# Optimization experiments

Hardware: AMD Instinct MI355X
Metric: run time of the kernel (lower is better)

The kernel has to match this reference:

```python
import jax, jax.numpy as jnp
import numpy as np

B, T, C = 2, 4096, 768
H = 12
HD = C // H  # 64

def setup_inputs() -> dict:
    key = jax.random.key(0)
    k1, k2, k3 = jax.random.split(key, 3)
    scale_in = 1.0 / np.sqrt(C)
    return {
        "x": jax.random.normal(k1, (B, T, C), dtype=jnp.float32),
        "w_qkv": jax.random.normal(k2, (C, 3 * C), dtype=jnp.float32) * scale_in,
        "b_qkv": jnp.zeros((3 * C,), dtype=jnp.float32),
        "w_proj": jax.random.normal(k3, (C, C), dtype=jnp.float32) * scale_in,
        "b_proj": jnp.zeros((C,), dtype=jnp.float32),
    }

def reference(x, w_qkv, b_qkv, w_proj, b_proj):
    # Dropout in eval mode (identity), matching module.eval().
    Bx, Tx, Cx = x.shape
    qkv = x @ w_qkv + b_qkv                      # [B,T,3C]
    q, k, v = jnp.split(qkv, 3, axis=-1)
    def to_heads(t):
        return t.reshape(Bx, Tx, H, HD).transpose(0, 2, 1, 3)  # [B,H,T,hd]
    q, k, v = to_heads(q), to_heads(k), to_heads(v)
    att = jnp.einsum('bhqd,bhkd->bhqk', q, k) / jnp.sqrt(jnp.float32(HD))
    causal = jnp.tril(jnp.ones((Tx, Tx), dtype=bool))
    att = jnp.where(causal[None, None], att, -jnp.inf)
    att = jax.nn.softmax(att, axis=-1)
    y = jnp.einsum('bhqk,bhkd->bhqd', att, v)    # [B,H,T,hd]
    y = y.transpose(0, 2, 1, 3).reshape(Bx, Tx, Cx)
    return y @ w_proj + b_proj
```

## Files before the change

### kernel.cpp

```cpp
#include <hip/hip_runtime.h>


#define TSEQ 4096
#define NH 12
#define CDIM 768

typedef __bf16 bf16;
typedef __attribute__((ext_vector_type(8))) __bf16 bf16x8;
typedef __attribute__((ext_vector_type(4))) __bf16 bf16x4;
typedef __attribute__((ext_vector_type(4))) float f32x4;

__device__ __forceinline__ void gload16(const void* g, void* l) {
  __builtin_amdgcn_global_load_lds(
      (const __attribute__((address_space(1))) void*)g,
      (__attribute__((address_space(3))) void*)l, 16, 0, 0);
}

__device__ __forceinline__ float fexp2(float x) {
  return __builtin_amdgcn_exp2f(x);
}

#define MAX3(a, b, c) fmaxf(fmaxf((a), (b)), (c))

__global__ void convert_x_kernel(const float* __restrict__ x,
                                 bf16* __restrict__ xb, int n) {
  int i = (blockIdx.x * blockDim.x + threadIdx.x) * 4;
  if (i < n) {
    float4 v = *(const float4*)(x + i);
    bf16x4 o;
    o[0] = (bf16)v.x; o[1] = (bf16)v.y; o[2] = (bf16)v.z; o[3] = (bf16)v.w;
    *(bf16x4*)(xb + i) = o;
  }
}

__global__ void transpose_w_kernel(const float* __restrict__ src,
                                   bf16* __restrict__ dst, int R, int Cc) {
  __shared__ float tile[32][33];
  int tx = threadIdx.x, ty = threadIdx.y;
  int c0 = blockIdx.x * 32, r0 = blockIdx.y * 32;
#pragma unroll
  for (int i = 0; i < 4; ++i)
    tile[ty + i * 8][tx] = src[(size_t)(r0 + ty + i * 8) * Cc + c0 + tx];
  __syncthreads();
#pragma unroll
  for (int i = 0; i < 4; ++i)
    dst[(size_t)(c0 + ty + i * 8) * R + r0 + tx] = (bf16)tile[tx][ty + i * 8];
}

template <int MODE>
__global__ __launch_bounds__(256) void gemm_kernel(
    const bf16* __restrict__ A, const bf16* __restrict__ BT,
    const float* __restrict__ bias, bf16* __restrict__ qk_out,
    bf16* __restrict__ vT_out, float* __restrict__ c_out) {
  constexpr int K = 768;
  __shared__ alignas(16) bf16 As[128 * 64];
  __shared__ alignas(16) bf16 Bs[128 * 64];
  const int t = threadIdx.x;
  const int l = t & 63, w = t >> 6;
  const int l15 = l & 15, lg = l >> 4;
  const int nwg = gridDim.x * gridDim.y;
  int id = blockIdx.y * gridDim.x + blockIdx.x;
  id = (id & 7) * (nwg >> 3) + (id >> 3);
  const int m0 = (id / gridDim.x) << 7, n0 = (id % gridDim.x) << 7;
  const int wr = w >> 1, wc = w & 1;

  f32x4 acc[4][4] = {};

  const int r0 = t >> 3;
  const int kb8 = (((t & 7) ^ (r0 & 7)) << 3);
  const bf16* Asrc = A + (size_t)(m0 + r0) * K + kb8;
  const bf16* Bsrc = BT + (size_t)(n0 + r0) * K + kb8;

  for (int kt = 0; kt < K / 64; ++kt) {
#pragma unroll
    for (int i = 0; i < 4; ++i)
      gload16(Asrc + kt * 64 + (size_t)i * 32 * K, (char*)As + w * 1024 + i * 4096);
#pragma unroll
    for (int i = 0; i < 4; ++i)
      gload16(Bsrc + kt * 64 + (size_t)i * 32 * K, (char*)Bs + w * 1024 + i * 4096);
    __syncthreads();
#pragma unroll
    for (int kk = 0; kk < 2; ++kk) {
      bf16x8 af[4], bfv[4];
#pragma unroll
      for (int m = 0; m < 4; ++m) {
        int r = (wr << 6) + (m << 4) + l15;
        int kb = (kk << 2) + lg;
        af[m] = *(const bf16x8*)((const char*)As + r * 128 + ((kb ^ (r & 7)) << 4));
      }
#pragma unroll
      for (int n = 0; n < 4; ++n) {
        int r = (wc << 6) + (n << 4) + l15;
        int kb = (kk << 2) + lg;
        bfv[n] = *(const bf16x8*)((const char*)Bs + r * 128 + ((kb ^ (r & 7)) << 4));
      }
#pragma unroll
      for (int m = 0; m < 4; ++m)
#pragma unroll
        for (int n = 0; n < 4; ++n)
          acc[m][n] = __builtin_amdgcn_mfma_f32_16x16x32_bf16(af[m], bfv[n],
                                                              acc[m][n], 0, 0, 0);
    }
    __syncthreads();
  }

#pragma unroll
  for (int m = 0; m < 4; ++m) {
    int row = m0 + (wr << 6) + (m << 4) + (lg << 2);
    int b = row >> 12, tt = row & 4095;
#pragma unroll
    for (int n = 0; n < 4; ++n) {
      int col = n0 + (wc << 6) + (n << 4) + l15;
      float bv = bias[col];
      if (MODE == 0) {
        if (col < 1536) {
          float sc = (col < 768) ? 0.18033688011112042f : 1.0f;
          bf16* dst = qk_out + (size_t)(b * TSEQ + tt) * 1536 + col;
#pragma unroll
          for (int j = 0; j < 4; ++j)
            dst[(size_t)j * 1536] = (bf16)((acc[m][n][j] + bv) * sc);
        } else {
          int nl = col - 1536;
          bf16* dst = vT_out +
              ((size_t)(b * NH + (nl >> 6)) * 64 + (nl & 63)) * TSEQ + tt;
#pragma unroll
          for (int j = 0; j < 4; ++j) dst[j] = (bf16)(acc[m][n][j] + bv);
        }
      } else {
        float* dst = c_out + (size_t)row * 768 + col;
#pragma unroll
        for (int j = 0; j < 4; ++j) dst[(size_t)j * 768] = acc[m][n][j] + bv;
      }
    }
  }
}

__global__ __launch_bounds__(256) void attn_kernel(
    const bf16* __restrict__ qk,
    const bf16* __restrict__ vT,
    bf16* __restrict__ y,
    bf16* __restrict__ opart,
    float* __restrict__ mlb) {
  __shared__ alignas(16) char lds[24576];
  const int t = threadIdx.x;
  const int l = t & 63, w = t >> 6;
  const int l15 = l & 15, lg = l >> 4;

  const int rk = blockIdx.x;
  const int xcd = rk & 7, s = rk >> 3;
  const int bh = xcd * 3 + (s % 3);
  const int j = s / 3;
  int qb, kt0, kt1, half, split;
  if (j < 64) {
    int i = j >> 1;
    qb = 63 - i; half = j & 1; split = 1;
    int nk = qb + 1, nh0 = (nk + 1) >> 1;
    kt0 = half ? nh0 : 0;
    kt1 = half ? nk : nh0;
  } else {
    qb = 95 - j; half = 0; split = 0;
    kt0 = 0; kt1 = qb + 1;
  }
  const int b = bh / NH, h = bh % NH;
  const bf16* qbase = qk + (size_t)b * TSEQ * 1536 + h * 64;
  const bf16* kbase = qbase + 768;
  const bf16* vbase = vT + (size_t)bh * 64 * TSEQ;

  const int r0 = t >> 3;
  const int kb8 = (((t & 7) ^ (r0 & 7)) << 3);
  const int q0 = qb << 6;
  const int qw = q0 + (w << 4);

  const int swz = l15 & 7;
  int koff[2];
  koff[0] = l15 * 128 + ((lg ^ swz) << 4);
  koff[1] = l15 * 128 + (((4 + lg) ^ swz) << 4);
  char* const preg = lds + w * 2048;
  const char* par[2] = {preg + koff[0], preg + koff[1]};
  char* pwa[4];
#pragma unroll
  for (int m = 0; m < 4; ++m)
    pwa[m] = preg + l15 * 128 + ((((m << 5) + (lg << 3)) ^ (swz << 4)));

#pragma unroll
  for (int i = 0; i < 2; ++i) {
    gload16(qbase + (size_t)(q0 + i * 32 + r0) * 1536 + kb8,
            lds + w * 1024 + i * 4096);
    gload16(kbase + (size_t)(kt0 * 64 + i * 32 + r0) * 1536 + kb8,
            lds + 0x2000 + w * 1024 + i * 4096);
    gload16(vbase + (size_t)(i * 32 + r0) * TSEQ + kt0 * 64 + kb8,
            lds + 0x4000 + w * 1024 + i * 4096);
  }
  const bf16* ksrc = kbase + (size_t)((kt0 + 1) * 64 + r0) * 1536 + kb8;
  const bf16* vsrc = vbase + (size_t)r0 * TSEQ + (kt0 + 1) * 64 + kb8;
  int4 kr0, kr1, vr0, vr1;
  if (kt0 + 1 < kt1) {
    kr0 = *(const int4*)(ksrc);
    kr1 = *(const int4*)(ksrc + (size_t)32 * 1536);
    vr0 = *(const int4*)(vsrc);
    vr1 = *(const int4*)(vsrc + (size_t)32 * TSEQ);
    ksrc += (size_t)64 * 1536;
    vsrc += 64;
  }
  __syncthreads();

  bf16x8 qf[2];
#pragma unroll
  for (int kk = 0; kk < 2; ++kk) {
    int r = (w << 4) + l15;
    int kb = (kk << 2) + lg;
    qf[kk] = *(const bf16x8*)(lds + r * 128 + ((kb ^ (r & 7)) << 4));
  }

  f32x4 o[4] = {};
  float mrun = -__builtin_inff();
  float lrun = 0.f;

  for (int kt = kt0; kt < kt1; ++kt) {
    const int kv0 = kt << 6;

    f32x4 s4[4] = {};
    __builtin_amdgcn_s_setprio(1);
#pragma unroll
    for (int kk = 0; kk < 2; ++kk) {
#pragma unroll
      for (int m = 0; m < 4; ++m) {
        bf16x8 kf = *(const bf16x8*)(lds + 0x2000 + koff[kk] + m * 2048);
        s4[m] = __builtin_amdgcn_mfma_f32_16x16x32_bf16(kf, qf[kk], s4[m], 0, 0, 0);
      }
    }
    __builtin_amdgcn_s_setprio(0);

    if (kv0 + 63 > qw) {
      int q = qw + l15;
#pragma unroll
      for (int m = 0; m < 4; ++m) {
        int kvr = kv0 + (m << 4) + (lg << 2);
#pragma unroll
        for (int jj = 0; jj < 4; ++jj)
          if (kvr + jj > q) s4[m][jj] = -__builtin_inff();
      }
    }
    float t0 = MAX3(s4[0][0], s4[0][1], s4[0][2]);
    float t1 = MAX3(s4[0][3], s4[1][0], s4[1][1]);
    float t2 = MAX3(s4[1][2], s4[1][3], s4[2][0]);
    float t3 = MAX3(s4[2][1], s4[2][2], s4[2][3]);
    float t4 = MAX3(s4[3][0], s4[3][1], s4[3][2]);
    float cmax = MAX3(MAX3(t0, t1, s4[3][3]), fmaxf(t2, t3), t4);
    cmax = fmaxf(cmax, __shfl_xor(cmax, 16));
    cmax = fmaxf(cmax, __shfl_xor(cmax, 32));
    if (__any(cmax > mrun + 8.f)) {
      float mnew = fmaxf(mrun, cmax);
      float alpha = fexp2(mrun - mnew);
      mrun = mnew;
      lrun *= alpha;
#pragma unroll
      for (int jj = 0; jj < 4; ++jj) {
        int rr = (lg << 2) + jj;
        float a = __shfl(alpha, (l & 48) | rr);
#pragma unroll
        for (int no = 0; no < 4; ++no) o[no][jj] *= a;
      }
    }
    float ps = 0.f;
#pragma unroll
    for (int m = 0; m < 4; ++m)
#pragma unroll
      for (int jj = 0; jj < 4; ++jj) {
        float pv = fexp2(s4[m][jj] - mrun);
        s4[m][jj] = pv;
        ps += pv;
      }
    ps += __shfl_xor(ps, 16);
    ps += __shfl_xor(ps, 32);
    lrun += ps;
#pragma unroll
    for (int m = 0; m < 4; ++m) {
      bf16x4 pv;
#pragma unroll
      for (int jj = 0; jj < 4; ++jj) pv[jj] = (bf16)s4[m][jj];
      *(bf16x4*)(pwa[m]) = pv;
    }
    __builtin_amdgcn_s_setprio(1);
#pragma unroll
    for (int kk = 0; kk < 2; ++kk) {
      bf16x8 pa = *(const bf16x8*)(par[kk]);
#pragma unroll
      for (int no = 0; no < 4; ++no) {
        bf16x8 vb = *(const bf16x8*)(lds + 0x4000 + koff[kk] + no * 2048);
        o[no] = __builtin_amdgcn_mfma_f32_16x16x32_bf16(pa, vb, o[no], 0, 0, 0);
      }
    }
    __builtin_amdgcn_s_setprio(0);

    if (kt + 1 < kt1) {
      __syncthreads();
      *(int4*)(lds + 0x2000 + t * 16) = kr0;
      *(int4*)(lds + 0x2000 + 4096 + t * 16) = kr1;
      *(int4*)(lds + 0x4000 + t * 16) = vr0;
      *(int4*)(lds + 0x4000 + 4096 + t * 16) = vr1;
      if (kt + 2 < kt1) {
        kr0 = *(const int4*)(ksrc);
        kr1 = *(const int4*)(ksrc + (size_t)32 * 1536);
        vr0 = *(const int4*)(vsrc);
        vr1 = *(const int4*)(vsrc + (size_t)32 * TSEQ);
        ksrc += (size_t)64 * 1536;
        vsrc += 64;
      }
      __syncthreads();
    }
  }

  if (!split) {
#pragma unroll
    for (int jj = 0; jj < 4; ++jj) {
      int rr = (lg << 2) + jj;
      float lv = __shfl(lrun, (l & 48) | rr);
      float linv = 1.0f / lv;
      int qrow = qw + rr;
      size_t base = ((size_t)(b * TSEQ + qrow)) * 768 + h * 64;
#pragma unroll
      for (int no = 0; no < 4; ++no)
        y[base + (no << 4) + l15] = (bf16)(o[no][jj] * linv);
    }
  } else {
    const int sb2 = (bh * 32 + (qb - 32)) * 2 + half;
#pragma unroll
    for (int jj = 0; jj < 4; ++jj) {
      int rr = (lg << 2) + jj;
      float lv = __shfl(lrun, (l & 48) | rr);
      float linv = 1.0f / lv;
      int r = (w << 4) + rr;
      size_t base = ((size_t)sb2 * 64 + r) * 64;
#pragma unroll
      for (int no = 0; no < 4; ++no)
        opart[base + (no << 4) + l15] = (bf16)(o[no][jj] * linv);
    }
    if (l < 16) {
      size_t mi = ((size_t)sb2 * 64 + (w << 4) + l) * 2;
      mlb[mi] = mrun;
      mlb[mi + 1] = lrun;
    }
  }
}

__global__ void combine_kernel(const bf16* __restrict__ op,
                               const float* __restrict__ ml,
                               bf16* __restrict__ y) {
  int g = blockIdx.x * 256 + threadIdx.x;
  int d4 = (g & 15) << 2;
  int rid = g >> 4;
  int rr = rid & 63;
  int sb = rid >> 6;
  int bh = sb >> 5, qb = 32 + (sb & 31);
  int b = bh / NH, h = bh % NH;
  size_t m0i = ((size_t)(sb * 2) * 64 + rr) * 2;
  size_t m1i = ((size_t)(sb * 2 + 1) * 64 + rr) * 2;
  float m0 = ml[m0i], l0 = ml[m0i + 1];
  float m1 = ml[m1i], l1 = ml[m1i + 1];
  float M = fmaxf(m0, m1);
  float w0 = fexp2(m0 - M) * l0, w1 = fexp2(m1 - M) * l1;
  float inv = 1.f / (w0 + w1);
  w0 *= inv; w1 *= inv;
  const bf16* o0 = op + (((size_t)(sb * 2) * 64 + rr) * 64 + d4);
  const bf16* o1 = op + (((size_t)(sb * 2 + 1) * 64 + rr) * 64 + d4);
  bf16x4 a = *(const bf16x4*)o0, c = *(const bf16x4*)o1;
  bf16x4 out;
#pragma unroll
  for (int jj = 0; jj < 4; ++jj)
    out[jj] = (bf16)(w0 * (float)a[jj] + w1 * (float)c[jj]);
  int qrow = (qb << 6) + rr;
  *(bf16x4*)(y + ((size_t)(b * TSEQ + qrow)) * 768 + h * 64 + d4) = out;
}

extern "C" void kernel_launch(void* const* d_in, const int* in_sizes, int n_in,
                              void* d_out, int out_size, void* d_ws,
                              size_t ws_size, hipStream_t stream) {
  const float* x = (const float*)d_in[0];
  const float* w_qkv = (const float*)d_in[1];
  const float* b_qkv = (const float*)d_in[2];
  const float* w_proj = (const float*)d_in[3];
  const float* b_proj = (const float*)d_in[4];
  float* out = (float*)d_out;
  char* ws = (char*)d_ws;

  bf16* xb     = (bf16*)(ws);
  bf16* wqkvT  = (bf16*)(ws + 12582912);
  bf16* wprojT = (bf16*)(ws + 16121856);
  bf16* qkbuf  = (bf16*)(ws + 17301504);
  bf16* vTbuf  = (bf16*)(ws + 42467328);
  bf16* ybuf   = (bf16*)(ws + 55050240);
  float* mlb   = (float*)(ws + 67633152);

  convert_x_kernel<<<6144, 256, 0, stream>>>(x, xb, 2 * TSEQ * CDIM);
  transpose_w_kernel<<<dim3(72, 24), dim3(32, 8), 0, stream>>>(w_qkv, wqkvT, 768, 2304);
  transpose_w_kernel<<<dim3(24, 24), dim3(32, 8), 0, stream>>>(w_proj, wprojT, 768, 768);
  gemm_kernel<0><<<dim3(18, 64), 256, 0, stream>>>(xb, wqkvT, b_qkv, qkbuf, vTbuf, nullptr);
  attn_kernel<<<2304, 256, 0, stream>>>(qkbuf, vTbuf, ybuf, xb, mlb);
  combine_kernel<<<3072, 256, 0, stream>>>(xb, mlb, ybuf);
  gemm_kernel<1><<<dim3(6, 64), 256, 0, stream>>>(ybuf, wprojT, b_proj, nullptr, nullptr, out);
}
```

Baseline: 247.7 us.

## Enlarge attention query tile to 128 rows with two 16-row subtiles per wave

After: 268.6 us. 8.4% more time.

```diff
diff --git a/kernel.cpp b/kernel.cpp
--- a/kernel.cpp
+++ b/kernel.cpp
@@ -135,13 +135,13 @@
   }
 }
 
-__global__ __launch_bounds__(256) void attn_kernel(
+__global__ __launch_bounds__(256, 4) void attn_kernel(
     const bf16* __restrict__ qk,
     const bf16* __restrict__ vT,
     bf16* __restrict__ y,
     bf16* __restrict__ opart,
     float* __restrict__ mlb) {
-  __shared__ alignas(16) char lds[24576];
+  __shared__ alignas(16) char lds[32768];
   const int t = threadIdx.x;
   const int l = t & 63, w = t >> 6;
   const int l15 = l & 15, lg = l >> 4;
@@ -151,15 +151,14 @@
   const int bh = xcd * 3 + (s % 3);
   const int j = s / 3;
   int qb, kt0, kt1, half, split;
-  if (j < 64) {
-    int i = j >> 1;
-    qb = 63 - i; half = j & 1; split = 1;
-    int nk = qb + 1, nh0 = (nk + 1) >> 1;
+  if (j < 32) {
+    qb = 31 - (j >> 1); half = j & 1; split = 1;
+    int nh0 = qb + 1;
     kt0 = half ? nh0 : 0;
-    kt1 = half ? nk : nh0;
+    kt1 = half ? 2 * qb + 2 : nh0;
   } else {
-    qb = 95 - j; half = 0; split = 0;
-    kt0 = 0; kt1 = qb + 1;
+    qb = 47 - j; half = 0; split = 0;
+    kt0 = 0; kt1 = 2 * qb + 2;
   }
   const int b = bh / NH, h = bh % NH;
   const bf16* qbase = qk + (size_t)b * TSEQ * 1536 + h * 64;
@@ -168,28 +167,29 @@
 
   const int r0 = t >> 3;
   const int kb8 = (((t & 7) ^ (r0 & 7)) << 3);
-  const int q0 = qb << 6;
-  const int qw = q0 + (w << 4);
+  const int q0 = qb << 7;
+  const int qwmax = q0 + (w << 5) + 31;
 
   const int swz = l15 & 7;
   int koff[2];
   koff[0] = l15 * 128 + ((lg ^ swz) << 4);
   koff[1] = l15 * 128 + (((4 + lg) ^ swz) << 4);
-  char* const preg = lds + w * 2048;
-  const char* par[2] = {preg + koff[0], preg + koff[1]};
-  char* pwa[4];
+  char* const preg = lds + w * 4096;
+  int so[4];
 #pragma unroll
   for (int m = 0; m < 4; ++m)
-    pwa[m] = preg + l15 * 128 + ((((m << 5) + (lg << 3)) ^ (swz << 4)));
-
-#pragma unroll
-  for (int i = 0; i < 2; ++i) {
+    so[m] = l15 * 128 + ((((m << 5) + (lg << 3)) ^ (swz << 4)));
+
+#pragma unroll
+  for (int i = 0; i < 4; ++i)
     gload16(qbase + (size_t)(q0 + i * 32 + r0) * 1536 + kb8,
             lds + w * 1024 + i * 4096);
+#pragma unroll
+  for (int i = 0; i < 2; ++i) {
     gload16(kbase + (size_t)(kt0 * 64 + i * 32 + r0) * 1536 + kb8,
-            lds + 0x2000 + w * 1024 + i * 4096);
+            lds + 0x4000 + w * 1024 + i * 4096);
     gload16(vbase + (size_t)(i * 32 + r0) * TSEQ + kt0 * 64 + kb8,
-            lds + 0x4000 + w * 1024 + i * 4096);
+            lds + 0x6000 + w * 1024 + i * 4096);
   }
   const bf16* ksrc = kbase + (size_t)((kt0 + 1) * 64 + r0) * 1536 + kb8;
   const bf16* vsrc = vbase + (size_t)r0 * TSEQ + (kt0 + 1) * 64 + kb8;
@@ -204,101 +204,137 @@
   }
   __syncthreads();
 
-  bf16x8 qf[2];
-#pragma unroll
-  for (int kk = 0; kk < 2; ++kk) {
-    int r = (w << 4) + l15;
-    int kb = (kk << 2) + lg;
-    qf[kk] = *(const bf16x8*)(lds + r * 128 + ((kb ^ (r & 7)) << 4));
-  }
-
-  f32x4 o[4] = {};
-  float mrun = -__builtin_inff();
-  float lrun = 0.f;
+  bf16x8 qf[2][2];
+#pragma unroll
+  for (int n = 0; n < 2; ++n)
+#pragma unroll
+    for (int kk = 0; kk < 2; ++kk) {
+      int r = (w << 5) + (n << 4) + l15;
+      int kb = (kk << 2) + lg;
+      qf[n][kk] = *(const bf16x8*)(lds + r * 128 + ((kb ^ (r & 7)) << 4));
+    }
+
+  f32x4 o[2][4] = {};
+  float mrun[2] = {0.f, 0.f};
+  float lrun[2] = {0.f, 0.f};
 
   for (int kt = kt0; kt < kt1; ++kt) {
     const int kv0 = kt << 6;
 
-    f32x4 s4[4] = {};
-    __builtin_amdgcn_s_setprio(1);
-#pragma unroll
-    for (int kk = 0; kk < 2; ++kk) {
-#pragma unroll
-      for (int m = 0; m < 4; ++m) {
-        bf16x8 kf = *(const bf16x8*)(lds + 0x2000 + koff[kk] + m * 2048);
-        s4[m] = __builtin_amdgcn_mfma_f32_16x16x32_bf16(kf, qf[kk], s4[m], 0, 0, 0);
-      }
-    }
-    __builtin_amdgcn_s_setprio(0);
-
-    if (kv0 + 63 > qw) {
-      int q = qw + l15;
-#pragma unroll
-      for (int m = 0; m < 4; ++m) {
-        int kvr = kv0 + (m << 4) + (lg << 2);
-#pragma unroll
-        for (int jj = 0; jj < 4; ++jj)
-          if (kvr + jj > q) s4[m][jj] = -__builtin_inff();
-      }
-    }
-    float t0 = MAX3(s4[0][0], s4[0][1], s4[0][2]);
-    float t1 = MAX3(s4[0][3], s4[1][0], s4[1][1]);
-    float t2 = MAX3(s4[1][2], s4[1][3], s4[2][0]);
-    float t3 = MAX3(s4[2][1], s4[2][2], s4[2][3]);
-    float t4 = MAX3(s4[3][0], s4[3][1], s4[3][2]);
-    float cmax = MAX3(MAX3(t0, t1, s4[3][3]), fmaxf(t2, t3), t4);
-    cmax = fmaxf(cmax, __shfl_xor(cmax, 16));
-    cmax = fmaxf(cmax, __shfl_xor(cmax, 32));
-    if (__any(cmax > mrun + 8.f)) {
-      float mnew = fmaxf(mrun, cmax);
-      float alpha = fexp2(mrun - mnew);
-      mrun = mnew;
-      lrun *= alpha;
-#pragma unroll
-      for (int jj = 0; jj < 4; ++jj) {
-        int rr = (lg << 2) + jj;
-        float a = __shfl(alpha, (l & 48) | rr);
-#pragma unroll
-        for (int no = 0; no < 4; ++no) o[no][jj] *= a;
-      }
-    }
-    float ps = 0.f;
-#pragma unroll
-    for (int m = 0; m < 4; ++m)
-#pragma unroll
-      for (int jj = 0; jj < 4; ++jj) {
-        float pv = fexp2(s4[m][jj] - mrun);
-        s4[m][jj] = pv;
-        ps += pv;
-      }
-    ps += __shfl_xor(ps, 16);
-    ps += __shfl_xor(ps, 32);
-    lrun += ps;
-#pragma unroll
-    for (int m = 0; m < 4; ++m) {
-      bf16x4 pv;
-#pragma unroll
-      for (int jj = 0; jj < 4; ++jj) pv[jj] = (bf16)s4[m][jj];
-      *(bf16x4*)(pwa[m]) = pv;
-    }
-    __builtin_amdgcn_s_setprio(1);
-#pragma unroll
-    for (int kk = 0; kk < 2; ++kk) {
-      bf16x8 pa = *(const bf16x8*)(par[kk]);
-#pragma unroll
-      for (int no = 0; no < 4; ++no) {
-        bf16x8 vb = *(const bf16x8*)(lds + 0x4000 + koff[kk] + no * 2048);
-        o[no] = __builtin_amdgcn_mfma_f32_16x16x32_bf16(pa, vb, o[no], 0, 0, 0);
-      }
-    }
-    __builtin_amdgcn_s_setprio(0);
+    if (kv0 <= qwmax) {
+      f32x4 s4[2][4];
+#pragma unroll
+      for (int n = 0; n < 2; ++n) {
+        float mi = -mrun[n];
+#pragma unroll
+        for (int m = 0; m < 4; ++m) {
+          s4[n][m][0] = mi; s4[n][m][1] = mi; s4[n][m][2] = mi; s4[n][m][3] = mi;
+        }
+      }
+      __builtin_amdgcn_s_setprio(1);
+#pragma unroll
+      for (int kk = 0; kk < 2; ++kk) {
+        bf16x8 kf[4];
+#pragma unroll
+        for (int m = 0; m < 4; ++m)
+          kf[m] = *(const bf16x8*)(lds + 0x4000 + koff[kk] + m * 2048);
+#pragma unroll
+        for (int m = 0; m < 4; ++m)
+#pragma unroll
+          for (int n = 0; n < 2; ++n)
+            s4[n][m] = __builtin_amdgcn_mfma_f32_16x16x32_bf16(
+                kf[m], qf[n][kk], s4[n][m], 0, 0, 0);
+      }
+      __builtin_amdgcn_s_setprio(0);
+
+      if (kv0 + 63 > q0 + (w << 5)) {
+#pragma unroll
+        for (int n = 0; n < 2; ++n) {
+          int qn = q0 + (w << 5) + (n << 4) + l15;
+#pragma unroll
+          for (int m = 0; m < 4; ++m) {
+            int kvr = kv0 + (m << 4) + (lg << 2);
+#pragma unroll
+            for (int jj = 0; jj < 4; ++jj)
+              if (kvr + jj > qn) s4[n][m][jj] = -__builtin_inff();
+          }
+        }
+      }
+      float cm[2];
+#pragma unroll
+      for (int n = 0; n < 2; ++n) {
+        float t0 = MAX3(s4[n][0][0], s4[n][0][1], s4[n][0][2]);
+        float t1 = MAX3(s4[n][0][3], s4[n][1][0], s4[n][1][1]);
+        float t2 = MAX3(s4[n][1][2], s4[n][1][3], s4[n][2][0]);
+        float t3 = MAX3(s4[n][2][1], s4[n][2][2], s4[n][2][3]);
+        float t4 = MAX3(s4[n][3][0], s4[n][3][1], s4[n][3][2]);
+        float c = MAX3(MAX3(t0, t1, s4[n][3][3]), fmaxf(t2, t3), t4);
+        c = fmaxf(c, __shfl_xor(c, 16));
+        cm[n] = fmaxf(c, __shfl_xor(c, 32));
+      }
+      if (__any((cm[0] > 8.f) || (cm[1] > 8.f))) {
+#pragma unroll
+        for (int n = 0; n < 2; ++n) {
+          float delta = fmaxf(cm[n], 0.f);
+          float alpha = fexp2(-delta);
+          mrun[n] += delta;
+          lrun[n] *= alpha;
+#pragma unroll
+          for (int jj = 0; jj < 4; ++jj) {
+            int rr = (lg << 2) + jj;
+            float a = __shfl(alpha, (l & 48) | rr);
+#pragma unroll
+            for (int no = 0; no < 4; ++no) o[n][no][jj] *= a;
+          }
+#pragma unroll
+          for (int m = 0; m < 4; ++m)
+#pragma unroll
+            for (int jj = 0; jj < 4; ++jj) s4[n][m][jj] -= delta;
+        }
+      }
+#pragma unroll
+      for (int n = 0; n < 2; ++n) {
+        float ps = 0.f;
+#pragma unroll
+        for (int m = 0; m < 4; ++m) {
+          bf16x4 pv;
+#pragma unroll
+          for (int jj = 0; jj < 4; ++jj) {
+            float p = fexp2(s4[n][m][jj]);
+            pv[jj] = (bf16)p;
+            ps += p;
+          }
+          *(bf16x4*)(preg + (n << 11) + so[m]) = pv;
+        }
+        ps += __shfl_xor(ps, 16);
+        ps += __shfl_xor(ps, 32);
+        lrun[n] += ps;
+      }
+      __builtin_amdgcn_s_setprio(1);
+#pragma unroll
+      for (int kk = 0; kk < 2; ++kk) {
+        bf16x8 vbv[4];
+#pragma unroll
+        for (int no = 0; no < 4; ++no)
+          vbv[no] = *(const bf16x8*)(lds + 0x6000 + koff[kk] + no * 2048);
+#pragma unroll
+        for (int n = 0; n < 2; ++n) {
+          bf16x8 pa = *(const bf16x8*)(preg + (n << 11) + koff[kk]);
+#pragma unroll
+          for (int no = 0; no < 4; ++no)
+            o[n][no] = __builtin_amdgcn_mfma_f32_16x16x32_bf16(
+                pa, vbv[no], o[n][no], 0, 0, 0);
+        }
+      }
+      __builtin_amdgcn_s_setprio(0);
+    }
 
     if (kt + 1 < kt1) {
       __syncthreads();
-      *(int4*)(lds + 0x2000 + t * 16) = kr0;
-      *(int4*)(lds + 0x2000 + 4096 + t * 16) = kr1;
-      *(int4*)(lds + 0x4000 + t * 16) = vr0;
-      *(int4*)(lds + 0x4000 + 4096 + t * 16) = vr1;
+      *(int4*)(lds + 0x4000 + t * 16) = kr0;
+      *(int4*)(lds + 0x4000 + 4096 + t * 16) = kr1;
+      *(int4*)(lds + 0x6000 + t * 16) = vr0;
+      *(int4*)(lds + 0x6000 + 4096 + t * 16) = vr1;
       if (kt + 2 < kt1) {
         kr0 = *(const int4*)(ksrc);
         kr1 = *(const int4*)(ksrc + (size_t)32 * 1536);
@@ -313,33 +349,40 @@
 
   if (!split) {
 #pragma unroll
-    for (int jj = 0; jj < 4; ++jj) {
-      int rr = (lg << 2) + jj;
-      float lv = __shfl(lrun, (l & 48) | rr);
-      float linv = 1.0f / lv;
-      int qrow = qw + rr;
-      size_t base = ((size_t)(b * TSEQ + qrow)) * 768 + h * 64;
-#pragma unroll
-      for (int no = 0; no < 4; ++no)
-        y[base + (no << 4) + l15] = (bf16)(o[no][jj] * linv);
-    }
+    for (int n = 0; n < 2; ++n)
+#pragma unroll
+      for (int jj = 0; jj < 4; ++jj) {
+        int rr = (lg << 2) + jj;
+        float lv = __shfl(lrun[n], (l & 48) | rr);
+        float linv = __builtin_amdgcn_rcpf(lv);
+        int qrow = q0 + (w << 5) + (n << 4) + rr;
+        size_t base = ((size_t)(b * TSEQ + qrow)) * 768 + h * 64;
+#pragma unroll
+        for (int no = 0; no < 4; ++no)
+          y[base + (no << 4) + l15] = (bf16)(o[n][no][jj] * linv);
+      }
   } else {
-    const int sb2 = (bh * 32 + (qb - 32)) * 2 + half;
-#pragma unroll
-    for (int jj = 0; jj < 4; ++jj) {
-      int rr = (lg << 2) + jj;
-      float lv = __shfl(lrun, (l & 48) | rr);
-      float linv = 1.0f / lv;
-      int r = (w << 4) + rr;
-      size_t base = ((size_t)sb2 * 64 + r) * 64;
-#pragma unroll
-      for (int no = 0; no < 4; ++no)
-        opart[base + (no << 4) + l15] = (bf16)(o[no][jj] * linv);
-    }
+    const int sb2 = (bh * 16 + (qb - 16)) * 2 + half;
+#pragma unroll
+    for (int n = 0; n < 2; ++n)
+#pragma unroll
+      for (int jj = 0; jj < 4; ++jj) {
+        int rr = (lg << 2) + jj;
+        float lv = __shfl(lrun[n], (l & 48) | rr);
+        float linv = __builtin_amdgcn_rcpf(lv);
+        int r = (w << 5) + (n << 4) + rr;
+        size_t base = ((size_t)sb2 * 128 + r) * 64;
+#pragma unroll
+        for (int no = 0; no < 4; ++no)
+          opart[base + (no << 4) + l15] = (bf16)(o[n][no][jj] * linv);
+      }
     if (l < 16) {
-      size_t mi = ((size_t)sb2 * 64 + (w << 4) + l) * 2;
-      mlb[mi] = mrun;
-      mlb[mi + 1] = lrun;
+#pragma unroll
+      for (int n = 0; n < 2; ++n) {
+        size_t mi = ((size_t)sb2 * 128 + (w << 5) + (n << 4) + l) * 2;
+        mlb[mi] = mrun[n];
+        mlb[mi + 1] = lrun[n];
+      }
     }
   }
 }
@@ -350,26 +393,26 @@
   int g = blockIdx.x * 256 + threadIdx.x;
   int d4 = (g & 15) << 2;
   int rid = g >> 4;
-  int rr = rid & 63;
-  int sb = rid >> 6;
-  int bh = sb >> 5, qb = 32 + (sb & 31);
+  int rr = rid & 127;
+  int sb = rid >> 7;
+  int bh = sb >> 4, qb = 16 + (sb & 15);
   int b = bh / NH, h = bh % NH;
-  size_t m0i = ((size_t)(sb * 2) * 64 + rr) * 2;
-  size_t m1i = ((size_t)(sb * 2 + 1) * 64 + rr) * 2;
+  size_t m0i = ((size_t)(sb * 2) * 128 + rr) * 2;
+  size_t m1i = ((size_t)(sb * 2 + 1) * 128 + rr) * 2;
   float m0 = ml[m0i], l0 = ml[m0i + 1];
   float m1 = ml[m1i], l1 = ml[m1i + 1];
   float M = fmaxf(m0, m1);
   float w0 = fexp2(m0 - M) * l0, w1 = fexp2(m1 - M) * l1;
   float inv = 1.f / (w0 + w1);
   w0 *= inv; w1 *= inv;
-  const bf16* o0 = op + (((size_t)(sb * 2) * 64 + rr) * 64 + d4);
-  const bf16* o1 = op + (((size_t)(sb * 2 + 1) * 64 + rr) * 64 + d4);
+  const bf16* o0 = op + (((size_t)(sb * 2) * 128 + rr) * 64 + d4);
+  const bf16* o1 = op + (((size_t)(sb * 2 + 1) * 128 + rr) * 64 + d4);
   bf16x4 a = *(const bf16x4*)o0, c = *(const bf16x4*)o1;
   bf16x4 out;
 #pragma unroll
   for (int jj = 0; jj < 4; ++jj)
     out[jj] = (bf16)(w0 * (float)a[jj] + w1 * (float)c[jj]);
-  int qrow = (qb << 6) + rr;
+  int qrow = (qb << 7) + rr;
   *(bf16x4*)(y + ((size_t)(b * TSEQ + qrow)) * 768 + h * 64 + d4) = out;
 }
 
@@ -396,7 +439,7 @@
   transpose_w_kernel<<<dim3(72, 24), dim3(32, 8), 0, stream>>>(w_qkv, wqkvT, 768, 2304);
   transpose_w_kernel<<<dim3(24, 24), dim3(32, 8), 0, stream>>>(w_proj, wprojT, 768, 768);
   gemm_kernel<0><<<dim3(18, 64), 256, 0, stream>>>(xb, wqkvT, b_qkv, qkbuf, vTbuf, nullptr);
-  attn_kernel<<<2304, 256, 0, stream>>>(qkbuf, vTbuf, ybuf, xb, mlb);
+  attn_kernel<<<1152, 256, 0, stream>>>(qkbuf, vTbuf, ybuf, xb, mlb);
   combine_kernel<<<3072, 256, 0, stream>>>(xb, mlb, ybuf);
   gemm_kernel<1><<<dim3(6, 64), 256, 0, stream>>>(ybuf, wprojT, b_proj, nullptr, nullptr, out);
 }
```
